# Kernel tuning notes

Hardware: AMD Instinct MI355X
Metric: run time of the kernel (lower is better)

The kernel has to match this reference:

```python
import jax, jax.numpy as jnp
import numpy as np

D_MODEL = 1024
N_HEAD = 8
STRIDE = 8
HEAD_DIM = D_MODEL // N_HEAD
NEG_INF = jnp.float32(-1e30)  # stand-in for -inf, safe under softmax


def setup_inputs() -> dict:
    key = jax.random.key(0)
    ks = jax.random.split(key, 8)
    B, TGT, SRC = 2, 1024, 8192
    scale = 1.0 / np.sqrt(D_MODEL)
    return {
        "q": jax.random.normal(ks[0], (B, TGT, D_MODEL), jnp.float32),
        "k": jax.random.normal(ks[1], (B, SRC, D_MODEL), jnp.float32),
        "v": jax.random.normal(ks[2], (B, SRC, D_MODEL), jnp.float32),
        "Wq": jax.random.normal(ks[3], (D_MODEL, D_MODEL), jnp.float32) * scale,
        "bq": jnp.zeros((D_MODEL,), jnp.float32),
        "Wk": jax.random.normal(ks[4], (D_MODEL, D_MODEL), jnp.float32) * scale,
        "bk": jnp.zeros((D_MODEL,), jnp.float32),
        "Wv": jax.random.normal(ks[5], (D_MODEL, D_MODEL), jnp.float32) * scale,
        "bv": jnp.zeros((D_MODEL,), jnp.float32),
        "Wo": jax.random.normal(ks[6], (D_MODEL, D_MODEL), jnp.float32) * scale,
        "bo": jnp.zeros((D_MODEL,), jnp.float32),
    }


def _hepos_head_mask(src_len):
    # mask_h[h, j] True where position j is DISALLOWED for head h:
    # (j - h) % stride != 0. If a head would mask everything, unmask j=0
    # (matches the torch fallback; cannot happen when n_head <= stride... it
    # can when h >= stride? here h < n_head <= stride handled generically).
    src_idx = jnp.arange(src_len)  # [src]
    h_idx = jnp.arange(N_HEAD)[:, None]  # [H,1]
    m = ((src_idx[None, :] - h_idx) % STRIDE) != 0  # [H, src]
    all_masked = jnp.all(m, axis=-1, keepdims=True)  # [H,1]
    m = m.at[:, 0].set(jnp.where(all_masked[:, 0], False, m[:, 0]))
    return m


def reference(q, k, v, Wq, bq, Wk, bk, Wv, bv, Wo, bo):
    B, tgt_len, _ = q.shape
    src_len = k.shape[1]
    # projections (torch Linear: x @ W^T + b; here W stored as [d_in, d_out])
    Q = (q @ Wq + bq).reshape(B, tgt_len, N_HEAD, HEAD_DIM)
    K = (k @ Wk + bk).reshape(B, src_len, N_HEAD, HEAD_DIM)
    V = (v @ Wv + bv).reshape(B, src_len, N_HEAD, HEAD_DIM)
    # dense scores [B, H, tgt, src]
    scores = jnp.einsum('bthd,bshd->bhts', Q, K) / np.sqrt(HEAD_DIM)
    head_mask = _hepos_head_mask(src_len)  # [H, src], True -> disallowed
    scores = jnp.where(head_mask[None, :, None, :], NEG_INF, scores)
    attn = jax.nn.softmax(scores, axis=-1)
    out = jnp.einsum('bhts,bshd->bthd', attn, V).reshape(B, tgt_len, D_MODEL)
    return out @ Wo + bo
```

## Files before the change

### kernel.cpp

```cpp
#include <hip/hip_runtime.h>
#include <hip/hip_bf16.h>
#include <stdint.h>

#define DM 1024
#define HD 128
#define NH 8
#define NB 2
#define TGT 1024
#define SRC 8192
#define JPH 1024
#define LOG2E 1.4426950408889634f

typedef __attribute__((ext_vector_type(8))) short bf16x8;
typedef __attribute__((ext_vector_type(4))) float f32x4;

__device__ __forceinline__ unsigned short f2bf(float f) {
  __hip_bfloat16 h = __float2bfloat16(f);
  return __builtin_bit_cast(unsigned short, h);
}

__device__ __forceinline__ void gload_lds16(const void* g, void* l) {
  __builtin_amdgcn_global_load_lds(
      (const __attribute__((address_space(1))) unsigned int*)g,
      (__attribute__((address_space(3))) unsigned int*)l, 16, 0, 0);
}

__global__ __launch_bounds__(256) void wconv_kernel(
    const float* __restrict__ Wq, const float* __restrict__ Wk,
    const float* __restrict__ Wv, const float* __restrict__ Wo,
    unsigned short* __restrict__ WTout) {
  __shared__ float tile[64][65];
  const float* W = (blockIdx.z == 0) ? Wq : (blockIdx.z == 1) ? Wk
                   : (blockIdx.z == 2) ? Wv : Wo;
  unsigned short* WT = WTout + (size_t)blockIdx.z * DM * DM;
  const int k0 = blockIdx.x * 64, n0 = blockIdx.y * 64;
  const int tid = threadIdx.x;
  const int tr = tid >> 4, tc = (tid & 15) * 4;
  for (int it = 0; it < 4; ++it) {
    int r = tr + it * 16;
    float4 vv = *(const float4*)(&W[(size_t)(k0 + r) * DM + n0 + tc]);
    tile[r][tc] = vv.x; tile[r][tc + 1] = vv.y;
    tile[r][tc + 2] = vv.z; tile[r][tc + 3] = vv.w;
  }
  __syncthreads();
  for (int it = 0; it < 4; ++it) {
    int n = tr + it * 16;
    ushort4 o;
    o.x = f2bf(tile[tc + 0][n]); o.y = f2bf(tile[tc + 1][n]);
    o.z = f2bf(tile[tc + 2][n]); o.w = f2bf(tile[tc + 3][n]);
    *(ushort4*)(&WT[(size_t)(n0 + n) * DM + k0 + tc]) = o;
  }
}

__global__ __launch_bounds__(256, 2) void proj_fused_kernel(
    const float* __restrict__ q, const float* __restrict__ k,
    const float* __restrict__ v, const unsigned short* __restrict__ WTall,
    const float* __restrict__ bq, const float* __restrict__ bk,
    const float* __restrict__ bv, unsigned short* __restrict__ Qp,
    unsigned short* __restrict__ Kp, unsigned short* __restrict__ VpT) {
  __shared__ unsigned short Ab[2][64 * 64];
  __shared__ unsigned short Bb[3][128 * 64];
  const int tid = threadIdx.x, lane = tid & 63, w = tid >> 6;
  const int wm = w >> 1, wn = w & 1;
  const int l15 = lane & 15, l4 = lane >> 4;

  const int bid = blockIdx.x;
  const int lbid = (bid & 7) * 96 + (bid >> 3);
  const int mode = lbid >> 8;
  const int sub = lbid & 255;
  const float* Asrc;
  const unsigned short* WT;
  const float* bias;
  int nbase, bh = 0, Mtile;
  if (mode == 0) {
    Asrc = q; WT = WTall; bias = bq;
    Mtile = sub >> 3; nbase = (sub & 7) * 128;
  } else {
    bh = sub >> 4; Mtile = sub & 15;
    nbase = (bh & 7) * 128;
    if (mode == 1) { Asrc = k; WT = WTall + (size_t)DM * DM; bias = bk; }
    else           { Asrc = v; WT = WTall + (size_t)2 * DM * DM; bias = bv; }
  }

  const int ar = tid >> 2;
  const int ac = (tid & 3) * 16;
  size_t growA;
  if (mode == 0) growA = (size_t)(Mtile * 64 + ar);
  else growA = (size_t)(bh >> 3) * SRC + (size_t)(bh & 7) +
               8u * (size_t)(Mtile * 64 + ar);
  const float* aptr = &Asrc[growA * DM + ac];

  auto issueA = [&](int t, float4 (&R)[4]) {
    const float* src = aptr + t * 64;
#pragma unroll
    for (int i = 0; i < 4; ++i) R[i] = *(const float4*)(src + i * 4);
  };
  auto commitA = [&](float4 (&R)[4], int buf) {
    unsigned char* abase = (unsigned char*)Ab[buf] + ar * 128;
#pragma unroll
    for (int h = 0; h < 2; ++h) {
      bf16x8 pk;
      float4 x = R[h * 2], y = R[h * 2 + 1];
      pk[0] = (short)f2bf(x.x); pk[1] = (short)f2bf(x.y);
      pk[2] = (short)f2bf(x.z); pk[3] = (short)f2bf(x.w);
      pk[4] = (short)f2bf(y.x); pk[5] = (short)f2bf(y.y);
      pk[6] = (short)f2bf(y.z); pk[7] = (short)f2bf(y.w);
      int b0 = (ac * 2 + h * 16) ^ ((ar & 7) << 4);
      *(bf16x8*)(abase + b0) = pk;
    }
  };
  auto stageB = [&](int t, int buf) {
    const int kk0 = t * 64;
    unsigned char* dst = (unsigned char*)Bb[buf];
#pragma unroll
    for (int it = 0; it < 4; ++it) {
      int gi = w * 4 + it;
      int row = gi * 8 + (lane >> 3);
      const unsigned char* g =
          (const unsigned char*)&WT[(size_t)(nbase + row) * DM + kk0];
      g += ((lane & 7) * 16) ^ ((row & 7) << 4);
      gload_lds16(g, dst + gi * 1024);
    }
  };

  f32x4 acc[2][4] = {};
  float4 aR0[4], aR1[4];

  issueA(0, aR0);
  stageB(0, 0);
  issueA(1, aR1);
  stageB(1, 1);
  commitA(aR0, 0);
  asm volatile("s_waitcnt vmcnt(8) lgkmcnt(0)" ::: "memory");
  __builtin_amdgcn_s_barrier();
  __builtin_amdgcn_sched_barrier(0);

  int bc = 0;

  auto body = [&](int T, float4 (&RC)[4], float4 (&RN)[4]) {
    int bp = bc + 2; if (bp >= 3) bp -= 3;
    if (T + 2 < 16) {
      issueA(T + 2, RC);
      stageB(T + 2, bp);
    }

    const unsigned char* Bbase = (const unsigned char*)Bb[0] + bc * 16384;
    const unsigned char* Abase = (const unsigned char*)Ab[T & 1];
    bf16x8 af[2][2], bfr[4][2];
#pragma unroll
    for (int kk = 0; kk < 2; ++kk) {
#pragma unroll
      for (int f = 0; f < 2; ++f) {
        int ra = wm * 32 + f * 16 + l15;
        int ka = (kk * 64 + l4 * 16) ^ ((ra & 7) << 4);
        af[f][kk] = *(const bf16x8*)(Abase + ra * 128 + ka);
      }
#pragma unroll
      for (int g = 0; g < 4; ++g) {
        int rb = wn * 64 + g * 16 + l15;
        int kb = (kk * 64 + l4 * 16) ^ ((rb & 7) << 4);
        bfr[g][kk] = *(const bf16x8*)(Bbase + rb * 128 + kb);
      }
    }
#pragma unroll
    for (int kk = 0; kk < 2; ++kk)
#pragma unroll
      for (int f = 0; f < 2; ++f)
#pragma unroll
        for (int g = 0; g < 4; ++g)
          acc[f][g] = __builtin_amdgcn_mfma_f32_16x16x32_bf16(
              af[f][kk], bfr[g][kk], acc[f][g], 0, 0, 0);

    if (T + 1 < 16) commitA(RN, (T + 1) & 1);

    if (T + 2 < 16)
      asm volatile("s_waitcnt vmcnt(8) lgkmcnt(0)" ::: "memory");
    else
      asm volatile("s_waitcnt vmcnt(0) lgkmcnt(0)" ::: "memory");
    __builtin_amdgcn_s_barrier();
    __builtin_amdgcn_sched_barrier(0);
    bc = bc + 1; if (bc >= 3) bc -= 3;
  };

  for (int tt = 0; tt < 16; tt += 2) {
    body(tt, aR0, aR1);
    body(tt + 1, aR1, aR0);
  }

#pragma unroll
  for (int f = 0; f < 2; ++f) {
#pragma unroll
    for (int g = 0; g < 4; ++g) {
      const int mloc = wm * 32 + f * 16 + l4 * 4;
      const int nloc = wn * 64 + g * 16 + l15;
      const float bs = bias[nbase + nloc];
      if (mode == 2) {
        const int d = nloc;
        const int jp = Mtile * 64 + mloc;
        ushort4 o;
        o.x = f2bf(acc[f][g][0] + bs); o.y = f2bf(acc[f][g][1] + bs);
        o.z = f2bf(acc[f][g][2] + bs); o.w = f2bf(acc[f][g][3] + bs);
        *(ushort4*)(&VpT[((size_t)bh * HD + d) * JPH + jp]) = o;
      } else if (mode == 1) {
        for (int i = 0; i < 4; ++i) {
          int jp = Mtile * 64 + mloc + i;
          Kp[((size_t)bh * JPH + jp) * HD + nloc] = f2bf(acc[f][g][i] + bs);
        }
      } else {
        for (int i = 0; i < 4; ++i) {
          int mg = Mtile * 64 + mloc + i;
          int bb = mg >> 10, tt2 = mg & 1023;
          int ng = nbase + nloc;
          int h = ng >> 7, d = ng & 127;
          Qp[(((size_t)bb * NH + h) * TGT + tt2) * HD + d] =
              f2bf((acc[f][g][i] + bs) * 0.08838834764831845f);
        }
      }
    }
  }
}

__global__ __launch_bounds__(256) void attn_kernel(
    const unsigned short* __restrict__ Qp, const unsigned short* __restrict__ Kp,
    const unsigned short* __restrict__ VpT, unsigned short* __restrict__ O) {
  __shared__ unsigned short Klds[2][64 * 128];
  __shared__ unsigned short Vlds[2][128 * 64];
  __shared__ unsigned short Plds[4 * 16 * 64];
  const int tid = threadIdx.x, lane = tid & 63, w = tid >> 6;
  const int bid = blockIdx.x;
  const int lbid = (bid & 7) * 32 + (bid >> 3);
  const int tq = lbid & 15, bh = lbid >> 4;
  const int T0 = tq * 64 + w * 16;
  const int l15 = lane & 15, l4 = lane >> 4;

  bf16x8 qf[4];
  {
    const unsigned short* qrow = &Qp[((size_t)bh * TGT + T0 + l15) * HD];
    for (int kf = 0; kf < 4; ++kf)
      qf[kf] = *(const bf16x8*)(&qrow[kf * 32 + l4 * 8]);
  }

  f32x4 acc_o[8] = {};
  float m_run = -INFINITY, l_run = 0.f;

  const unsigned short* kbh = Kp + (size_t)bh * JPH * HD;
  const unsigned short* vbh = VpT + (size_t)bh * HD * JPH;

  auto stage = [&](int jt, int buf) {
    const int j0 = jt * 64;
#pragma unroll
    for (int it = 0; it < 4; ++it) {
      int rb = w * 16 + it * 4;
      int row = rb + l4;
      const unsigned char* g =
          (const unsigned char*)(kbh + (size_t)(j0 + row) * HD);
      g += (l15 * 16) ^ ((row & 7) << 4);
      gload_lds16(g, &Klds[buf][rb * 128]);
    }
#pragma unroll
    for (int it = 0; it < 4; ++it) {
      int rb = w * 32 + it * 8;
      int d = rb + (lane >> 3);
      const unsigned char* g =
          (const unsigned char*)(vbh + (size_t)d * JPH + j0);
      g += ((lane & 7) * 16) ^ ((d & 7) << 4);
      gload_lds16(g, &Vlds[buf][rb * 64]);
    }
  };

  stage(0, 0);
  asm volatile("s_waitcnt vmcnt(0)" ::: "memory");
  __builtin_amdgcn_s_barrier();
  __builtin_amdgcn_sched_barrier(0);

  for (int jt = 0; jt < 16; ++jt) {
    const int cb = jt & 1;
    if (jt < 15) stage(jt + 1, cb ^ 1);

    f32x4 acc_s[4] = {};
    for (int jf = 0; jf < 4; ++jf) {
      const int j = jf * 16 + l15;
      for (int kf = 0; kf < 4; ++kf) {
        int byteoff = (j * 256 + (kf * 32 + l4 * 8) * 2) ^ ((j & 7) << 4);
        bf16x8 kfr = *(const bf16x8*)((const unsigned char*)Klds[cb] + byteoff);
        acc_s[jf] = __builtin_amdgcn_mfma_f32_16x16x32_bf16(
            kfr, qf[kf], acc_s[jf], 0, 0, 0);
      }
    }

    float pmax = -INFINITY;
    for (int jf = 0; jf < 4; ++jf)
      for (int i = 0; i < 4; ++i) pmax = fmaxf(pmax, acc_s[jf][i]);
    pmax = fmaxf(pmax, __shfl_xor(pmax, 16, 64));
    pmax = fmaxf(pmax, __shfl_xor(pmax, 32, 64));
    const float m_new = fmaxf(m_run, pmax);
    const float alpha = exp2f((m_run - m_new) * LOG2E);
    float psum = 0.f;
    for (int jf = 0; jf < 4; ++jf) {
      float p0 = exp2f((acc_s[jf][0] - m_new) * LOG2E);
      float p1 = exp2f((acc_s[jf][1] - m_new) * LOG2E);
      float p2 = exp2f((acc_s[jf][2] - m_new) * LOG2E);
      float p3 = exp2f((acc_s[jf][3] - m_new) * LOG2E);
      psum += (p0 + p1) + (p2 + p3);
      ushort4 pk;
      pk.x = f2bf(p0); pk.y = f2bf(p1); pk.z = f2bf(p2); pk.w = f2bf(p3);
      int byteoff = (w * 2048 + l15 * 128 + (jf * 16 + l4 * 4) * 2) ^ ((l15 & 7) << 4);
      *(ushort4*)((unsigned char*)Plds + byteoff) = pk;
    }
    psum += __shfl_xor(psum, 16, 64);
    psum += __shfl_xor(psum, 32, 64);
    l_run = l_run * alpha + psum;
    m_run = m_new;

    float alphar[4];
    for (int i = 0; i < 4; ++i)
      alphar[i] = __shfl(alpha, (lane & 48) | (l4 * 4 + i), 64);
    for (int df = 0; df < 8; ++df) {
      acc_o[df][0] *= alphar[0]; acc_o[df][1] *= alphar[1];
      acc_o[df][2] *= alphar[2]; acc_o[df][3] *= alphar[3];
    }

    for (int kf2 = 0; kf2 < 2; ++kf2) {
      int poff = (w * 2048 + l15 * 128 + (kf2 * 32 + l4 * 8) * 2) ^ ((l15 & 7) << 4);
      bf16x8 pf = *(const bf16x8*)((const unsigned char*)Plds + poff);
      for (int df = 0; df < 8; ++df) {
        int d = df * 16 + l15;
        int voff = (d * 128 + (kf2 * 32 + l4 * 8) * 2) ^ ((d & 7) << 4);
        bf16x8 vf = *(const bf16x8*)((const unsigned char*)Vlds[cb] + voff);
        acc_o[df] = __builtin_amdgcn_mfma_f32_16x16x32_bf16(
            pf, vf, acc_o[df], 0, 0, 0);
      }
    }

    asm volatile("s_waitcnt vmcnt(0)" ::: "memory");
    __builtin_amdgcn_s_barrier();
    __builtin_amdgcn_sched_barrier(0);
  }

  const float li = 1.0f / l_run;
  float linv[4];
  for (int i = 0; i < 4; ++i)
    linv[i] = __shfl(li, (lane & 48) | (l4 * 4 + i), 64);

  const int b = bh >> 3, h = bh & 7;
  for (int df = 0; df < 8; ++df)
    for (int i = 0; i < 4; ++i) {
      int t = T0 + l4 * 4 + i;
      int d = df * 16 + l15;
      O[((size_t)b * TGT + t) * DM + h * HD + d] = f2bf(acc_o[df][i] * linv[i]);
    }
}

__global__ __launch_bounds__(256) void oproj_kernel(
    const unsigned short* __restrict__ Oin, const unsigned short* __restrict__ WoT,
    const float* __restrict__ bo, float* __restrict__ out) {
  __shared__ unsigned short Ab[2][64 * 64];
  __shared__ unsigned short Bb[2][128 * 64];
  const int tid = threadIdx.x, lane = tid & 63, w = tid >> 6;
  const int wm = w >> 1, wn = w & 1;
  const int n0 = blockIdx.x * 128, m0 = blockIdx.y * 64;
  const int l15 = lane & 15, l4 = lane >> 4;

  auto stageA = [&](int t, int buf) {
    const int kk0 = t * 64;
#pragma unroll
    for (int it = 0; it < 2; ++it) {
      int gi = w * 2 + it;
      int row = gi * 8 + (lane >> 3);
      const unsigned char* g =
          (const unsigned char*)&Oin[(size_t)(m0 + row) * DM + kk0];
      g += ((lane & 7) * 16) ^ ((row & 7) << 4);
      gload_lds16(g, (unsigned char*)Ab[buf] + gi * 1024);
    }
  };
  auto stageB = [&](int t, int buf) {
    const int kk0 = t * 64;
#pragma unroll
    for (int it = 0; it < 4; ++it) {
      int gi = w * 4 + it;
      int row = gi * 8 + (lane >> 3);
      const unsigned char* g =
          (const unsigned char*)&WoT[(size_t)(n0 + row) * DM + kk0];
      g += ((lane & 7) * 16) ^ ((row & 7) << 4);
      gload_lds16(g, (unsigned char*)Bb[buf] + gi * 1024);
    }
  };

  f32x4 acc[2][4] = {};
  stageA(0, 0);
  stageB(0, 0);
  asm volatile("s_waitcnt vmcnt(0)" ::: "memory");
  __builtin_amdgcn_s_barrier();
  __builtin_amdgcn_sched_barrier(0);

  for (int t = 0; t < 16; ++t) {
    const int cur = t & 1;
    if (t < 15) { stageA(t + 1, cur ^ 1); stageB(t + 1, cur ^ 1); }

    bf16x8 af[2][2], bfr[4][2];
#pragma unroll
    for (int kk = 0; kk < 2; ++kk) {
#pragma unroll
      for (int f = 0; f < 2; ++f) {
        int ra = wm * 32 + f * 16 + l15;
        int ka = (kk * 64 + l4 * 16) ^ ((ra & 7) << 4);
        af[f][kk] = *(const bf16x8*)((const unsigned char*)Ab[cur] + ra * 128 + ka);
      }
#pragma unroll
      for (int g = 0; g < 4; ++g) {
        int rb = wn * 64 + g * 16 + l15;
        int kb = (kk * 64 + l4 * 16) ^ ((rb & 7) << 4);
        bfr[g][kk] = *(const bf16x8*)((const unsigned char*)Bb[cur] + rb * 128 + kb);
      }
    }
#pragma unroll
    for (int kk = 0; kk < 2; ++kk)
#pragma unroll
      for (int f = 0; f < 2; ++f)
#pragma unroll
        for (int g = 0; g < 4; ++g)
          acc[f][g] = __builtin_amdgcn_mfma_f32_16x16x32_bf16(
              af[f][kk], bfr[g][kk], acc[f][g], 0, 0, 0);

    asm volatile("s_waitcnt vmcnt(0) lgkmcnt(0)" ::: "memory");
    __builtin_amdgcn_s_barrier();
    __builtin_amdgcn_sched_barrier(0);
  }

#pragma unroll
  for (int f = 0; f < 2; ++f)
#pragma unroll
    for (int g = 0; g < 4; ++g) {
      int nn = n0 + wn * 64 + g * 16 + l15;
      float bs = bo[nn];
      for (int i = 0; i < 4; ++i) {
        int mm = m0 + wm * 32 + f * 16 + l4 * 4 + i;
        out[(size_t)mm * DM + nn] = acc[f][g][i] + bs;
      }
    }
}

extern "C" void kernel_launch(void* const* d_in, const int* in_sizes, int n_in,
                              void* d_out, int out_size, void* d_ws,
                              size_t ws_size, hipStream_t stream) {
  const float* q  = (const float*)d_in[0];
  const float* k  = (const float*)d_in[1];
  const float* v  = (const float*)d_in[2];
  const float* Wq = (const float*)d_in[3];
  const float* bq = (const float*)d_in[4];
  const float* Wk = (const float*)d_in[5];
  const float* bk = (const float*)d_in[6];
  const float* Wv = (const float*)d_in[7];
  const float* bv = (const float*)d_in[8];
  const float* Wo = (const float*)d_in[9];
  const float* bo = (const float*)d_in[10];
  float* out = (float*)d_out;

  unsigned short* WT  = (unsigned short*)d_ws;
  unsigned short* Qp  = WT + (size_t)4 * DM * DM;
  unsigned short* Kp  = Qp + (size_t)2 * DM * DM;
  unsigned short* VpT = Kp + (size_t)2 * DM * DM;
  unsigned short* Obf = VpT + (size_t)2 * DM * DM;

  hipLaunchKernelGGL(wconv_kernel, dim3(16, 16, 4), dim3(256), 0, stream,
                     Wq, Wk, Wv, Wo, WT);
  hipLaunchKernelGGL(proj_fused_kernel, dim3(768), dim3(256), 0, stream,
                     q, k, v, WT, bq, bk, bv, Qp, Kp, VpT);
  hipLaunchKernelGGL(attn_kernel, dim3(256), dim3(256), 0, stream,
                     Qp, Kp, VpT, Obf);
  hipLaunchKernelGGL(oproj_kernel, dim3(8, 32), dim3(256), 0, stream,
                     Obf, WT + (size_t)3 * DM * DM, bo, out);
}
```

Before: 106.2 us.

## Drop LDS staging in projection GEMM, load fragments directly from global

The projection kernel no longer stages A and B tiles through shared memory with a triple-buffered async pipeline. Each wave now reads its fp32 activation rows and bf16 weight fragments straight from global memory into registers, converts them, and issues MFMAs. The tile shape becomes 128x64 with each wave owning 32 rows, and the occupancy hint rises to 3 blocks per CU. This removes LDS traffic and barriers, but it gives up cross-wave data reuse and software prefetching, so it depends on cache hits and uncoalesced per-lane loads.

```diff
diff --git a/kernel.cpp b/kernel.cpp
--- a/kernel.cpp
+++ b/kernel.cpp
@@ -52,16 +52,13 @@
   }
 }
 
-__global__ __launch_bounds__(256, 2) void proj_fused_kernel(
+__global__ __launch_bounds__(256, 3) void proj_fused_kernel(
     const float* __restrict__ q, const float* __restrict__ k,
     const float* __restrict__ v, const unsigned short* __restrict__ WTall,
     const float* __restrict__ bq, const float* __restrict__ bk,
     const float* __restrict__ bv, unsigned short* __restrict__ Qp,
     unsigned short* __restrict__ Kp, unsigned short* __restrict__ VpT) {
-  __shared__ unsigned short Ab[2][64 * 64];
-  __shared__ unsigned short Bb[3][128 * 64];
   const int tid = threadIdx.x, lane = tid & 63, w = tid >> 6;
-  const int wm = w >> 1, wn = w & 1;
   const int l15 = lane & 15, l4 = lane >> 4;
 
   const int bid = blockIdx.x;
@@ -74,94 +71,67 @@
   int nbase, bh = 0, Mtile;
   if (mode == 0) {
     Asrc = q; WT = WTall; bias = bq;
-    Mtile = sub >> 3; nbase = (sub & 7) * 128;
+    Mtile = sub >> 4; nbase = (sub & 15) * 64;
   } else {
-    bh = sub >> 4; Mtile = sub & 15;
-    nbase = (bh & 7) * 128;
+    bh = sub >> 4;
+    const int r = sub & 15;
+    Mtile = r >> 1;
+    nbase = (bh & 7) * 128 + (r & 1) * 64;
     if (mode == 1) { Asrc = k; WT = WTall + (size_t)DM * DM; bias = bk; }
     else           { Asrc = v; WT = WTall + (size_t)2 * DM * DM; bias = bv; }
   }
 
-  const int ar = tid >> 2;
-  const int ac = (tid & 3) * 16;
-  size_t growA;
-  if (mode == 0) growA = (size_t)(Mtile * 64 + ar);
-  else growA = (size_t)(bh >> 3) * SRC + (size_t)(bh & 7) +
-               8u * (size_t)(Mtile * 64 + ar);
-  const float* aptr = &Asrc[growA * DM + ac];
-
-  auto issueA = [&](int t, float4 (&R)[4]) {
-    const float* src = aptr + t * 64;
-#pragma unroll
-    for (int i = 0; i < 4; ++i) R[i] = *(const float4*)(src + i * 4);
-  };
-  auto commitA = [&](float4 (&R)[4], int buf) {
-    unsigned char* abase = (unsigned char*)Ab[buf] + ar * 128;
-#pragma unroll
-    for (int h = 0; h < 2; ++h) {
-      bf16x8 pk;
-      float4 x = R[h * 2], y = R[h * 2 + 1];
-      pk[0] = (short)f2bf(x.x); pk[1] = (short)f2bf(x.y);
-      pk[2] = (short)f2bf(x.z); pk[3] = (short)f2bf(x.w);
-      pk[4] = (short)f2bf(y.x); pk[5] = (short)f2bf(y.y);
-      pk[6] = (short)f2bf(y.z); pk[7] = (short)f2bf(y.w);
-      int b0 = (ac * 2 + h * 16) ^ ((ar & 7) << 4);
-      *(bf16x8*)(abase + b0) = pk;
-    }
-  };
-  auto stageB = [&](int t, int buf) {
-    const int kk0 = t * 64;
-    unsigned char* dst = (unsigned char*)Bb[buf];
-#pragma unroll
-    for (int it = 0; it < 4; ++it) {
-      int gi = w * 4 + it;
-      int row = gi * 8 + (lane >> 3);
-      const unsigned char* g =
-          (const unsigned char*)&WT[(size_t)(nbase + row) * DM + kk0];
-      g += ((lane & 7) * 16) ^ ((row & 7) << 4);
-      gload_lds16(g, dst + gi * 1024);
-    }
-  };
+  const int mrow = Mtile * 128 + w * 32 + l15;
+  const float* aA[2];
+  if (mode == 0) {
+    aA[0] = Asrc + (size_t)mrow * DM;
+    aA[1] = Asrc + (size_t)(mrow + 16) * DM;
+  } else {
+    const size_t base = (size_t)(bh >> 3) * SRC + (size_t)(bh & 7);
+    aA[0] = Asrc + (base + 8u * (size_t)mrow) * DM;
+    aA[1] = Asrc + (base + 8u * (size_t)(mrow + 16)) * DM;
+  }
+  const unsigned short* bB[4];
+#pragma unroll
+  for (int g = 0; g < 4; ++g)
+    bB[g] = WT + (size_t)(nbase + g * 16 + l15) * DM;
+
+  const int klane = l4 * 8;
 
   f32x4 acc[2][4] = {};
-  float4 aR0[4], aR1[4];
-
-  issueA(0, aR0);
-  stageB(0, 0);
-  issueA(1, aR1);
-  stageB(1, 1);
-  commitA(aR0, 0);
-  asm volatile("s_waitcnt vmcnt(8) lgkmcnt(0)" ::: "memory");
-  __builtin_amdgcn_s_barrier();
-  __builtin_amdgcn_sched_barrier(0);
-
-  int bc = 0;
-
-  auto body = [&](int T, float4 (&RC)[4], float4 (&RN)[4]) {
-    int bp = bc + 2; if (bp >= 3) bp -= 3;
-    if (T + 2 < 16) {
-      issueA(T + 2, RC);
-      stageB(T + 2, bp);
-    }
-
-    const unsigned char* Bbase = (const unsigned char*)Bb[0] + bc * 16384;
-    const unsigned char* Abase = (const unsigned char*)Ab[T & 1];
-    bf16x8 af[2][2], bfr[4][2];
-#pragma unroll
-    for (int kk = 0; kk < 2; ++kk) {
-#pragma unroll
-      for (int f = 0; f < 2; ++f) {
-        int ra = wm * 32 + f * 16 + l15;
-        int ka = (kk * 64 + l4 * 16) ^ ((ra & 7) << 4);
-        af[f][kk] = *(const bf16x8*)(Abase + ra * 128 + ka);
-      }
-#pragma unroll
-      for (int g = 0; g < 4; ++g) {
-        int rb = wn * 64 + g * 16 + l15;
-        int kb = (kk * 64 + l4 * 16) ^ ((rb & 7) << 4);
-        bfr[g][kk] = *(const bf16x8*)(Bbase + rb * 128 + kb);
-      }
-    }
+
+#pragma unroll
+  for (int t = 0; t < 16; ++t) {
+    const int k0 = t * 64 + klane;
+    float4 a32[2][2][2];
+    bf16x8 bfv[4][2];
+#pragma unroll
+    for (int f = 0; f < 2; ++f)
+#pragma unroll
+      for (int kk = 0; kk < 2; ++kk) {
+        const float* p = aA[f] + k0 + kk * 32;
+        a32[f][kk][0] = *(const float4*)(p);
+        a32[f][kk][1] = *(const float4*)(p + 4);
+      }
+#pragma unroll
+    for (int g = 0; g < 4; ++g)
+#pragma unroll
+      for (int kk = 0; kk < 2; ++kk)
+        bfv[g][kk] = *(const bf16x8*)(bB[g] + k0 + kk * 32);
+
+    bf16x8 af[2][2];
+#pragma unroll
+    for (int f = 0; f < 2; ++f)
+#pragma unroll
+      for (int kk = 0; kk < 2; ++kk) {
+        const float4 x = a32[f][kk][0], y = a32[f][kk][1];
+        bf16x8 pk;
+        pk[0] = (short)f2bf(x.x); pk[1] = (short)f2bf(x.y);
+        pk[2] = (short)f2bf(x.z); pk[3] = (short)f2bf(x.w);
+        pk[4] = (short)f2bf(y.x); pk[5] = (short)f2bf(y.y);
+        pk[6] = (short)f2bf(y.z); pk[7] = (short)f2bf(y.w);
+        af[f][kk] = pk;
+      }
 #pragma unroll
     for (int kk = 0; kk < 2; ++kk)
 #pragma unroll
@@ -169,46 +139,32 @@
 #pragma unroll
         for (int g = 0; g < 4; ++g)
           acc[f][g] = __builtin_amdgcn_mfma_f32_16x16x32_bf16(
-              af[f][kk], bfr[g][kk], acc[f][g], 0, 0, 0);
-
-    if (T + 1 < 16) commitA(RN, (T + 1) & 1);
-
-    if (T + 2 < 16)
-      asm volatile("s_waitcnt vmcnt(8) lgkmcnt(0)" ::: "memory");
-    else
-      asm volatile("s_waitcnt vmcnt(0) lgkmcnt(0)" ::: "memory");
-    __builtin_amdgcn_s_barrier();
-    __builtin_amdgcn_sched_barrier(0);
-    bc = bc + 1; if (bc >= 3) bc -= 3;
-  };
-
-  for (int tt = 0; tt < 16; tt += 2) {
-    body(tt, aR0, aR1);
-    body(tt + 1, aR1, aR0);
+              af[f][kk], bfv[g][kk], acc[f][g], 0, 0, 0);
   }
 
 #pragma unroll
   for (int f = 0; f < 2; ++f) {
 #pragma unroll
     for (int g = 0; g < 4; ++g) {
-      const int mloc = wm * 32 + f * 16 + l4 * 4;
-      const int nloc = wn * 64 + g * 16 + l15;
+      const int mloc = w * 32 + f * 16 + l4 * 4;
+      const int nloc = g * 16 + l15;
       const float bs = bias[nbase + nloc];
       if (mode == 2) {
-        const int d = nloc;
-        const int jp = Mtile * 64 + mloc;
+        const int d = nbase - (bh & 7) * 128 + nloc;
+        const int jp = Mtile * 128 + mloc;
         ushort4 o;
         o.x = f2bf(acc[f][g][0] + bs); o.y = f2bf(acc[f][g][1] + bs);
         o.z = f2bf(acc[f][g][2] + bs); o.w = f2bf(acc[f][g][3] + bs);
         *(ushort4*)(&VpT[((size_t)bh * HD + d) * JPH + jp]) = o;
       } else if (mode == 1) {
+        const int d = nbase - (bh & 7) * 128 + nloc;
         for (int i = 0; i < 4; ++i) {
-          int jp = Mtile * 64 + mloc + i;
-          Kp[((size_t)bh * JPH + jp) * HD + nloc] = f2bf(acc[f][g][i] + bs);
+          int jp = Mtile * 128 + mloc + i;
+          Kp[((size_t)bh * JPH + jp) * HD + d] = f2bf(acc[f][g][i] + bs);
         }
       } else {
         for (int i = 0; i < 4; ++i) {
-          int mg = Mtile * 64 + mloc + i;
+          int mg = Mtile * 128 + mloc + i;
           int bb = mg >> 10, tt2 = mg & 1023;
           int ng = nbase + nloc;
           int h = ng >> 7, d = ng & 127;
```

New measurement: 169.3 us. 1.6x slower.
